# Kernel optimization log

Hardware: AMD Instinct MI355X
Metric: run time of the kernel (lower is better)

Reference implementation:

```python
import jax, jax.numpy as jnp
import numpy as np

NBINS = 256
EARLY_STOP = 0.1  # fraction of nbins with no improvement before early break


def setup_inputs() -> dict:
    key = jax.random.key(0)
    x = jax.random.uniform(key, (8, 3, 1024, 1024), dtype=jnp.float32)
    return {"x": x}


def _otsu_forward(x):
    orig_shape = x.shape
    b, c, h, w = x.shape
    rows = b * c
    xf = x.reshape(rows, h * w)                      # (R, N) one image per row
    N = xf.shape[1]

    # Per-row shift so each row starts at 0 (mirrors `x = (x.T - min_value).T`).
    min_val = xf.min(axis=1, keepdims=True)          # (R, 1)
    xs = xf - min_val
    gmax = xs.max()                                  # global min of xs is 0, global max here
    edges = jnp.linspace(jnp.zeros((), xs.dtype), gmax, NBINS + 1)
    width = gmax / NBINS

    # Per-row histogram with torch.histc semantics over global [0, gmax].
    bin_idx = jnp.clip(jnp.floor(xs / width).astype(jnp.int32), 0, NBINS - 1)
    flat_idx = (jnp.arange(rows, dtype=jnp.int32)[:, None] * NBINS + bin_idx).reshape(-1)
    hist = jnp.bincount(flat_idx, length=rows * NBINS).reshape(rows, NBINS).astype(xs.dtype)
    cum_count = jnp.cumsum(hist, axis=1)             # px_bellow after each bin
    w0 = cum_count / N
    w1 = 1.0 - w0

    # Sorted prefix moments -> subset variances for every threshold in one pass.
    xsort = jnp.sort(xs, axis=1)
    row_mean = xs.mean(axis=1, keepdims=True)
    cvals = xsort - row_mean                         # variance is shift-invariant; centering for stability
    s1 = jnp.cumsum(cvals, axis=1)
    s2 = jnp.cumsum(cvals * cvals, axis=1)
    tot1 = s1[:, -1:]
    tot2 = s2[:, -1:]

    thresh = edges[1:]                               # bin_edges[bin+1], shape (NBINS,)
    # n0[r, bin] = #{xs[r] <= thresh[bin]}  (condition `x <= thresh` in the loop)
    n0 = jax.vmap(lambda row: jnp.searchsorted(row, thresh, side="right"))(xsort)  # (R, NBINS)

    def subset_var(S1, S2, n):
        # unbiased variance (torch.var default); nan for n <= 1 like torch
        nf = n.astype(xs.dtype)
        var = (S2 - S1 * S1 / jnp.maximum(nf, 1.0)) / jnp.maximum(nf - 1.0, 1.0)
        return jnp.where(n > 1, var, jnp.nan)

    idx0 = jnp.maximum(n0 - 1, 0)
    S1_0 = jnp.where(n0 > 0, jnp.take_along_axis(s1, idx0, axis=1), 0.0)
    S2_0 = jnp.where(n0 > 0, jnp.take_along_axis(s2, idx0, axis=1), 0.0)
    mu0 = subset_var(S1_0, S2_0, n0)                 # var of pixels <= thresh
    n1 = N - n0
    mu1 = subset_var(tot1 - S1_0, tot2 - S2_0, n1)   # var of pixels > thresh
    icv = w0 * w1 * (mu0 - mu1) ** 2                 # (R, NBINS)

    # Sequential argmax with the original's global early-stop counter.
    max_try = int(NBINS * EARLY_STOP)

    def step(carry, inputs):
        max_icv, best, no_upd, stopped = carry
        icv_b, t_b = inputs                          # (R,), scalar
        upd = (icv_b > max_icv) & jnp.logical_not(stopped)   # nan > x is False, as in torch
        max_icv = jnp.where(upd, icv_b, max_icv)
        best = jnp.where(upd, t_b, best)
        no_upd = jnp.where(jnp.any(upd), 0, no_upd + 1)
        stopped = stopped | (no_upd >= max_try)
        return (max_icv, best, no_upd, stopped), None

    init = (
        jnp.zeros(rows, xs.dtype),
        jnp.zeros(rows, xs.dtype),
        jnp.zeros((), jnp.int32),
        jnp.zeros((), jnp.bool_),
    )
    (_, best_thresh, _, _), _ = jax.lax.scan(step, init, (icv.T, thresh))

    final_thresh = best_thresh[:, None] + min_val    # back to original scale
    out = jnp.where(xf < final_thresh, jnp.zeros((), xs.dtype), xf)
    return out.reshape(orig_shape)


def reference(x):
    return _otsu_forward(x)
```

## Files before the change

### kernel.cpp

```cpp
#include <hip/hip_runtime.h>
#include <stdint.h>


#define ROWS 24
#define NPIX (1 << 20)
#define NBINS 256
#define BPR 64
#define CHUNK (NPIX / BPR)
#define MAX_TRY 25

typedef float f32x4 __attribute__((ext_vector_type(4)));

static constexpr double kMagic = 6755399441055744.0;
static constexpr double kD1Scale = 17592186044416.0;
static constexpr double kD1Inv = 1.0 / 17592186044416.0;
static constexpr double kD2Scale = 4503599627370496.0;
static constexpr double kD2Inv = 1.0 / 4503599627370496.0;
static constexpr double Nd = 1048576.0;
static constexpr double kEps = 1e-9;

#define OFF_PART  0
#define OFF_FINAL 12288
#define OFF_T32   12544
#define OFF_CNT   16384
#define OFF_COR   40960
#define OFF_D1    65536
#define OFF_D2    114688
#define WS_END    163840

__device__ __forceinline__ void reduce_minmax(const uint2* __restrict__ part,
                                              unsigned* lmn, unsigned* lmx,
                                              int nthreads) {
  int t = threadIdx.x;
  if (t < ROWS) { lmn[t] = 0xFFFFFFFFu; lmx[t] = 0u; }
  __syncthreads();
  for (int p = t; p < ROWS * BPR; p += nthreads) {
    uint2 v = part[p];
    atomicMin(&lmn[p >> 6], v.x);
    atomicMax(&lmx[p >> 6], v.y);
  }
  __syncthreads();
}

__device__ __forceinline__ double compute_w(const unsigned* lmn,
                                            const unsigned* lmx, int t) {
  double d = 0.0;
  if (t < ROWS)
    d = (double)__uint_as_float(lmx[t]) - (double)__uint_as_float(lmn[t]);
  for (int o = 16; o; o >>= 1) d = fmax(d, __shfl_down(d, o));
  return d / 256.0;
}

__global__ __launch_bounds__(256) void k_minmax(const float* __restrict__ x,
                                                uint2* __restrict__ part,
                                                uint4* __restrict__ zero_base) {
  int blk = blockIdx.x;
  if (blk < 36) {
    uint4 z; z.x = 0u; z.y = 0u; z.z = 0u; z.w = 0u;
    zero_base[blk * 256 + threadIdx.x] = z;
  }
  int row = blk / BPR, sub = blk % BPR;
  const float4* p = (const float4*)(x + (size_t)row * NPIX + (size_t)sub * CHUNK);
  float mn = 3.4e38f, mx = 0.0f;
  for (int i = threadIdx.x; i < CHUNK / 4; i += 256) {
    float4 v = p[i];
    mn = fminf(mn, fminf(fminf(v.x, v.y), fminf(v.z, v.w)));
    mx = fmaxf(mx, fmaxf(fmaxf(v.x, v.y), fmaxf(v.z, v.w)));
  }
  __shared__ float smn[4], smx[4];
  for (int o = 32; o; o >>= 1) {
    mn = fminf(mn, __shfl_down(mn, o));
    mx = fmaxf(mx, __shfl_down(mx, o));
  }
  int wave = threadIdx.x >> 6;
  if ((threadIdx.x & 63) == 0) { smn[wave] = mn; smx[wave] = mx; }
  __syncthreads();
  if (threadIdx.x == 0) {
    for (int w = 1; w < 4; ++w) { mn = fminf(mn, smn[w]); mx = fmaxf(mx, smx[w]); }
    uint2 r; r.x = __float_as_uint(mn); r.y = __float_as_uint(mx);
    part[blk] = r;
  }
}

__global__ __launch_bounds__(256) void k_hist(const float* __restrict__ x,
    const uint2* __restrict__ part,
    unsigned* __restrict__ gcnt, int* __restrict__ gcor,
    unsigned long long* __restrict__ gD1, unsigned long long* __restrict__ gD2) {
  __shared__ unsigned lmn[ROWS], lmx[ROWS];
  __shared__ unsigned long long hA[NBINS], hB[NBINS];
  __shared__ int hcor[NBINS];
  __shared__ double s_w, s_rmin;
  int t = threadIdx.x;
  int row = blockIdx.x / BPR, sub = blockIdx.x % BPR;
  hA[t] = 0ull; hB[t] = 0ull; hcor[t] = 0;
  reduce_minmax(part, lmn, lmx, 256);
  if (t < 32) {
    double wv = compute_w(lmn, lmx, t);
    if (t == 0) { s_w = wv; s_rmin = (double)__uint_as_float(lmn[row]); }
  }
  __syncthreads();
  double w = s_w, rmin = s_rmin, rw = 1.0 / w;
  const float4* p = (const float4*)(x + (size_t)row * NPIX + (size_t)sub * CHUNK);
  for (int i = t; i < CHUNK / 4; i += 256) {
    float4 v = p[i];
    float vv[4] = {v.x, v.y, v.z, v.w};
#pragma unroll
    for (int c = 0; c < 4; ++c) {
      double xs = (double)vv[c] - rmin;
      double q1 = xs * rw;
      int b = (int)q1;
      double fr = q1 - (double)b;
      int j; double off;
      if (__builtin_expect(fr >= kEps && fr <= 1.0 - kEps && b <= 255, 1)) {
        j = b; off = (double)b * w;
      } else {
        double q = xs / w;
        b = (int)q; if (b > 255) b = 255;
        double elo = (double)b * w, ehi = (double)(b + 1) * w;
        j = b; off = elo;
        if (xs > ehi) { if (b < 255) { j = b + 1; off = ehi; } }
        else if (b > 0 && xs <= elo) { j = b - 1; off = (double)j * w; }
        if (j != b) { atomicAdd(&hcor[b], 1); atomicAdd(&hcor[j], -1); }
      }
      double delta = xs - off;
      double t1 = fma(delta, kD1Scale, kMagic);
      double dd = delta * delta;
      double t2 = fma(dd, kD2Scale, kMagic);
      unsigned long long d1 = (unsigned long long)__double_as_longlong(t1)
                              & 0x0007FFFFFFFFFFFFull;
      unsigned long long d2 = (unsigned long long)__double_as_longlong(t2)
                              & 0x0007FFFFFFFFFFFFull;
      atomicAdd(&hA[j], d1 | (1ull << 44));
      atomicAdd(&hB[j], d2);
    }
  }
  __syncthreads();
  unsigned long long a = hA[t];
  unsigned c = (unsigned)(a >> 44);
  int base = row * NBINS + t;
  if (c) {
    atomicAdd(&gcnt[base], c);
    atomicAdd(&gD1[base], a & ((1ull << 44) - 1ull));
  }
  if (hB[t]) atomicAdd(&gD2[base], hB[t]);
  if (hcor[t]) atomicAdd(&gcor[base], hcor[t]);
}

__global__ __launch_bounds__(1024) void k_icv_scan(
    const unsigned* __restrict__ gcnt, const int* __restrict__ gcor,
    const unsigned long long* __restrict__ gD1,
    const unsigned long long* __restrict__ gD2,
    const uint2* __restrict__ part,
    double* __restrict__ finalt, float* __restrict__ t32g) {
  __shared__ unsigned lmn[ROWS], lmx[ROWS];
  __shared__ unsigned long long umask[ROWS][4];
  __shared__ unsigned long long ganyw[4];
  __shared__ double s_w;
  __shared__ int s_tstop;
  int t = threadIdx.x;
  if (t < 4) ganyw[t] = 0ull;
  if (t < ROWS * 4) ((unsigned long long*)umask)[t] = 0ull;
  reduce_minmax(part, lmn, lmx, 1024);
  if (t < 32) {
    double wv = compute_w(lmn, lmx, t);
    if (t == 0) s_w = wv;
  }
  __syncthreads();
  double w = s_w;
  int wave = t >> 6, lane = t & 63;
  const double dNAN = __builtin_nan("");

  for (int pass = 0; pass < 2; ++pass) {
    if (pass == 1 && wave >= 8) break;
    int r = pass ? 16 + wave : wave;
    double e1[4], e2[4];
    unsigned long long pc0[4];
#pragma unroll
    for (int k = 0; k < 4; ++k) {
      int bin = k * 64 + lane;
      int idx = r * NBINS + bin;
      unsigned n = gcnt[idx];
      int cor = gcor[idx];
      double d1 = (double)gD1[idx] * kD1Inv;
      double d2v = (double)gD2[idx] * kD2Inv;
      double elo = (double)bin * w;
      e1[k] = (double)n * elo + d1;
      e2[k] = (double)n * (elo * elo) + 2.0 * elo * d1 + d2v;
      pc0[k] = (unsigned long long)n |
               ((unsigned long long)(unsigned)(n + (unsigned)cor) << 32);
    }
    double c1 = 0.0, c2 = 0.0;
    unsigned long long cc = 0ull;
    double E1[4], E2[4];
    unsigned long long CC[4];
#pragma unroll
    for (int k = 0; k < 4; ++k) {
      double p1 = e1[k], p2 = e2[k];
      unsigned long long pc = pc0[k];
      for (int o = 1; o < 64; o <<= 1) {
        double u1 = __shfl_up(p1, o), u2 = __shfl_up(p2, o);
        unsigned long long uc = __shfl_up(pc, o);
        if (lane >= o) { p1 += u1; p2 += u2; pc += uc; }
      }
      E1[k] = p1 + c1; E2[k] = p2 + c2; CC[k] = pc + cc;
      c1 += __shfl(p1, 63); c2 += __shfl(p2, 63); cc += __shfl(pc, 63);
    }
    double total1 = c1, total2 = c2;
    double mean = total1 / Nd;
    double tot1 = total1 - Nd * mean;
    double tot2 = total2 - Nd * mean * mean;
    double icv4[4];
#pragma unroll
    for (int k = 0; k < 4; ++k) {
      unsigned n0i = (unsigned)(CC[k] & 0xffffffffull);
      double n0 = (double)n0i;
      double n1 = Nd - n0;
      double s1raw = E1[k], s2raw = E2[k];
      double S1 = s1raw - n0 * mean;
      double S2 = s2raw - 2.0 * mean * s1raw + n0 * mean * mean;
      double mu0 = (n0i > 1u) ? (S2 - S1 * S1 / n0) / (n0 - 1.0) : dNAN;
      double S1b = tot1 - S1, S2b = tot2 - S2;
      double mu1 = (n1 > 1.0) ? (S2b - S1b * S1b / n1) / (n1 - 1.0) : dNAN;
      double w0 = (double)(unsigned)(CC[k] >> 32) / Nd, w1v = 1.0 - w0;
      double ddv = mu0 - mu1;
      icv4[k] = w0 * w1v * ddv * ddv;
    }
    double m = 0.0;
    unsigned long long myMask[4];
#pragma unroll
    for (int k = 0; k < 4; ++k) {
      double v = icv4[k];
      double pm = v;
      for (int o = 1; o < 64; o <<= 1) {
        double u = __shfl_up(pm, o);
        if (lane >= o) pm = fmax(pm, u);
      }
      double excl = __shfl_up(pm, 1);
      double Mprev = (lane == 0) ? m : fmax(m, excl);
      bool upd = v > Mprev;
      myMask[k] = __ballot(upd);
      m = fmax(m, __shfl(pm, 63));
    }
    if (lane == 0) {
#pragma unroll
      for (int k = 0; k < 4; ++k) {
        umask[r][k] = myMask[k];
        atomicOr(&ganyw[k], myMask[k]);
      }
    }
  }
  __syncthreads();
  if (t == 0) {
    int no_upd = 0, tstop = 255;
    for (int b = 0; b < 256; ++b) {
      bool any = (ganyw[b >> 6] >> (b & 63)) & 1ull;
      if (any) no_upd = 0; else ++no_upd;
      if (no_upd >= MAX_TRY) { tstop = b; break; }
    }
    s_tstop = tstop;
  }
  __syncthreads();
  if (t < ROWS) {
    int tstop = s_tstop;
    int tbest = -1;
    for (int k = 3; k >= 0; --k) {
      unsigned long long msk = umask[t][k];
      int hi = k * 64 + 63;
      if (hi > tstop) {
        int shift = tstop - k * 64;
        if (shift < 0) msk = 0ull;
        else msk &= (shift >= 63) ? ~0ull : ((2ull << shift) - 1ull);
      }
      if (msk) { tbest = k * 64 + 63 - __clzll(msk); break; }
    }
    double rmin = (double)__uint_as_float(lmn[t]);
    double ft = (tbest >= 0) ? (double)(tbest + 1) * w + rmin : rmin;
    finalt[t] = ft;
    float f = (float)ft;
    if ((double)f < ft) f = __uint_as_float(__float_as_uint(f) + 1u);
    t32g[t] = f;
  }
}

__global__ __launch_bounds__(256) void k_out(const float* __restrict__ x,
                                             const float* __restrict__ t32g,
                                             float* __restrict__ out) {
  size_t i = (size_t)blockIdx.x * blockDim.x + threadIdx.x;
  size_t stride = (size_t)gridDim.x * blockDim.x;
  const f32x4* xin = (const f32x4*)x;
  f32x4* o = (f32x4*)out;
  size_t n4 = (size_t)ROWS * NPIX / 4;
  for (; i < n4; i += stride) {
    float ft = t32g[i >> 18];
    f32x4 v = xin[i];
    f32x4 rr;
    rr.x = (v.x < ft) ? 0.0f : v.x;
    rr.y = (v.y < ft) ? 0.0f : v.y;
    rr.z = (v.z < ft) ? 0.0f : v.z;
    rr.w = (v.w < ft) ? 0.0f : v.w;
    __builtin_nontemporal_store(rr, &o[i]);
  }
}

extern "C" void kernel_launch(void* const* d_in, const int* in_sizes, int n_in,
                              void* d_out, int out_size, void* d_ws, size_t ws_size,
                              hipStream_t stream) {
  const float* x = (const float*)d_in[0];
  float* out = (float*)d_out;
  char* ws = (char*)d_ws;
  uint2* part = (uint2*)(ws + OFF_PART);
  double* finalt = (double*)(ws + OFF_FINAL);
  float* t32g = (float*)(ws + OFF_T32);
  unsigned* gcnt = (unsigned*)(ws + OFF_CNT);
  int* gcor = (int*)(ws + OFF_COR);
  unsigned long long* gD1 = (unsigned long long*)(ws + OFF_D1);
  unsigned long long* gD2 = (unsigned long long*)(ws + OFF_D2);

  k_minmax<<<ROWS * BPR, 256, 0, stream>>>(x, part, (uint4*)(ws + OFF_CNT));
  k_hist<<<ROWS * BPR, 256, 0, stream>>>(x, part, gcnt, gcor, gD1, gD2);
  k_icv_scan<<<1, 1024, 0, stream>>>(gcnt, gcor, gD1, gD2, part, finalt, t32g);
  k_out<<<3072, 256, 0, stream>>>(x, t32g, out);
}
```

Baseline: 118.1 us.

## Fuse ICV scan into histogram kernel via last-block ticket, privatize LDS histograms

Removes the separate single-block k_icv_scan launch: the last histogram block (detected through a global atomic done-counter) runs the threshold scan with 256 threads over six row passes. The LDS histograms are replicated per wave to cut atomic contention, the fast-path bin test computes delta directly with an fma, and the output kernel grid shrinks to 2048 blocks. The tail now runs on fewer threads inside a kernel with its own occupancy limits, and correctness depends on the extra zeroed counter and on the fences being ordered correctly.

```diff
diff --git a/kernel.cpp b/kernel.cpp
--- a/kernel.cpp
+++ b/kernel.cpp
@@ -7,6 +7,7 @@
 #define NBINS 256
 #define BPR 64
 #define CHUNK (NPIX / BPR)
+#define NBLK (ROWS * BPR)
 #define MAX_TRY 25
 
 typedef float f32x4 __attribute__((ext_vector_type(4)));
@@ -17,16 +18,22 @@
 static constexpr double kD2Scale = 4503599627370496.0;
 static constexpr double kD2Inv = 1.0 / 4503599627370496.0;
 static constexpr double Nd = 1048576.0;
-static constexpr double kEps = 1e-9;
 
 #define OFF_PART  0
-#define OFF_FINAL 12288
-#define OFF_T32   12544
+#define OFF_T32   12288
 #define OFF_CNT   16384
 #define OFF_COR   40960
 #define OFF_D1    65536
 #define OFF_D2    114688
-#define WS_END    163840
+#define OFF_DONE  163840
+#define ZERO_END  167936
+
+__device__ __forceinline__ unsigned ldg_u32(const unsigned* p) {
+  return __hip_atomic_load(p, __ATOMIC_RELAXED, __HIP_MEMORY_SCOPE_AGENT);
+}
+__device__ __forceinline__ unsigned long long ldg_u64(const unsigned long long* p) {
+  return __hip_atomic_load(p, __ATOMIC_RELAXED, __HIP_MEMORY_SCOPE_AGENT);
+}
 
 __device__ __forceinline__ void reduce_minmax(const uint2* __restrict__ part,
                                               unsigned* lmn, unsigned* lmx,
@@ -34,7 +41,7 @@
   int t = threadIdx.x;
   if (t < ROWS) { lmn[t] = 0xFFFFFFFFu; lmx[t] = 0u; }
   __syncthreads();
-  for (int p = t; p < ROWS * BPR; p += nthreads) {
+  for (int p = t; p < NBLK; p += nthreads) {
     uint2 v = part[p];
     atomicMin(&lmn[p >> 6], v.x);
     atomicMax(&lmx[p >> 6], v.y);
@@ -55,7 +62,7 @@
                                                 uint2* __restrict__ part,
                                                 uint4* __restrict__ zero_base) {
   int blk = blockIdx.x;
-  if (blk < 36) {
+  if (blk < 37) {
     uint4 z; z.x = 0u; z.y = 0u; z.z = 0u; z.w = 0u;
     zero_base[blk * 256 + threadIdx.x] = z;
   }
@@ -82,25 +89,31 @@
   }
 }
 
-__global__ __launch_bounds__(256) void k_hist(const float* __restrict__ x,
+__global__ __launch_bounds__(256, 4) void k_hist(const float* __restrict__ x,
     const uint2* __restrict__ part,
     unsigned* __restrict__ gcnt, int* __restrict__ gcor,
-    unsigned long long* __restrict__ gD1, unsigned long long* __restrict__ gD2) {
+    unsigned long long* __restrict__ gD1, unsigned long long* __restrict__ gD2,
+    unsigned* __restrict__ gdone, float* __restrict__ t32g) {
   __shared__ unsigned lmn[ROWS], lmx[ROWS];
-  __shared__ unsigned long long hA[NBINS], hB[NBINS];
+  __shared__ unsigned long long hA[4][NBINS], hB[4][NBINS];
   __shared__ int hcor[NBINS];
   __shared__ double s_w, s_rmin;
   int t = threadIdx.x;
   int row = blockIdx.x / BPR, sub = blockIdx.x % BPR;
-  hA[t] = 0ull; hB[t] = 0ull; hcor[t] = 0;
+  int wavei = t >> 6, lane = t & 63;
+#pragma unroll
+  for (int wv = 0; wv < 4; ++wv) { hA[wv][t] = 0ull; hB[wv][t] = 0ull; }
+  hcor[t] = 0;
   reduce_minmax(part, lmn, lmx, 256);
-  if (t < 32) {
+  if (t < 64) {
     double wv = compute_w(lmn, lmx, t);
     if (t == 0) { s_w = wv; s_rmin = (double)__uint_as_float(lmn[row]); }
   }
   __syncthreads();
   double w = s_w, rmin = s_rmin, rw = 1.0 / w;
+  double lo_eps = w * 1e-9, hi_eps = w * (1.0 - 1e-9);
   const float4* p = (const float4*)(x + (size_t)row * NPIX + (size_t)sub * CHUNK);
+#pragma unroll 2
   for (int i = t; i < CHUNK / 4; i += 256) {
     float4 v = p[i];
     float vv[4] = {v.x, v.y, v.z, v.w};
@@ -109,81 +122,68 @@
       double xs = (double)vv[c] - rmin;
       double q1 = xs * rw;
       int b = (int)q1;
-      double fr = q1 - (double)b;
-      int j; double off;
-      if (__builtin_expect(fr >= kEps && fr <= 1.0 - kEps && b <= 255, 1)) {
-        j = b; off = (double)b * w;
-      } else {
+      double delta = fma(-(double)b, w, xs);
+      int j = b;
+      if (__builtin_expect(!(delta >= lo_eps) | !(delta <= hi_eps) | (b > 255), 0)) {
         double q = xs / w;
         b = (int)q; if (b > 255) b = 255;
         double elo = (double)b * w, ehi = (double)(b + 1) * w;
-        j = b; off = elo;
+        j = b; double off = elo;
         if (xs > ehi) { if (b < 255) { j = b + 1; off = ehi; } }
         else if (b > 0 && xs <= elo) { j = b - 1; off = (double)j * w; }
         if (j != b) { atomicAdd(&hcor[b], 1); atomicAdd(&hcor[j], -1); }
-      }
-      double delta = xs - off;
+        delta = xs - off;
+      }
       double t1 = fma(delta, kD1Scale, kMagic);
-      double dd = delta * delta;
-      double t2 = fma(dd, kD2Scale, kMagic);
+      double t2 = fma(delta * delta, kD2Scale, kMagic);
       unsigned long long d1 = (unsigned long long)__double_as_longlong(t1)
                               & 0x0007FFFFFFFFFFFFull;
       unsigned long long d2 = (unsigned long long)__double_as_longlong(t2)
                               & 0x0007FFFFFFFFFFFFull;
-      atomicAdd(&hA[j], d1 | (1ull << 44));
-      atomicAdd(&hB[j], d2);
-    }
-  }
-  __syncthreads();
-  unsigned long long a = hA[t];
+      atomicAdd(&hA[wavei][j], d1 | (1ull << 44));
+      atomicAdd(&hB[wavei][j], d2);
+    }
+  }
+  __syncthreads();
+  unsigned long long a = hA[0][t] + hA[1][t] + hA[2][t] + hA[3][t];
+  unsigned long long b2 = hB[0][t] + hB[1][t] + hB[2][t] + hB[3][t];
   unsigned c = (unsigned)(a >> 44);
   int base = row * NBINS + t;
   if (c) {
     atomicAdd(&gcnt[base], c);
     atomicAdd(&gD1[base], a & ((1ull << 44) - 1ull));
   }
-  if (hB[t]) atomicAdd(&gD2[base], hB[t]);
+  if (b2) atomicAdd(&gD2[base], b2);
   if (hcor[t]) atomicAdd(&gcor[base], hcor[t]);
-}
-
-__global__ __launch_bounds__(1024) void k_icv_scan(
-    const unsigned* __restrict__ gcnt, const int* __restrict__ gcor,
-    const unsigned long long* __restrict__ gD1,
-    const unsigned long long* __restrict__ gD2,
-    const uint2* __restrict__ part,
-    double* __restrict__ finalt, float* __restrict__ t32g) {
-  __shared__ unsigned lmn[ROWS], lmx[ROWS];
+
+  __threadfence();
+  __syncthreads();
+  __shared__ unsigned s_last;
+  if (t == 0) s_last = (atomicAdd(gdone, 1u) == NBLK - 1) ? 1u : 0u;
+  __syncthreads();
+  if (!s_last) return;
+  __threadfence();
+
   __shared__ unsigned long long umask[ROWS][4];
   __shared__ unsigned long long ganyw[4];
-  __shared__ double s_w;
   __shared__ int s_tstop;
-  int t = threadIdx.x;
   if (t < 4) ganyw[t] = 0ull;
-  if (t < ROWS * 4) ((unsigned long long*)umask)[t] = 0ull;
-  reduce_minmax(part, lmn, lmx, 1024);
-  if (t < 32) {
-    double wv = compute_w(lmn, lmx, t);
-    if (t == 0) s_w = wv;
-  }
-  __syncthreads();
-  double w = s_w;
-  int wave = t >> 6, lane = t & 63;
+  __syncthreads();
   const double dNAN = __builtin_nan("");
-
-  for (int pass = 0; pass < 2; ++pass) {
-    if (pass == 1 && wave >= 8) break;
-    int r = pass ? 16 + wave : wave;
+  double wv2 = s_w;
+  for (int pass = 0; pass < 6; ++pass) {
+    int r = pass * 4 + wavei;
     double e1[4], e2[4];
     unsigned long long pc0[4];
 #pragma unroll
     for (int k = 0; k < 4; ++k) {
       int bin = k * 64 + lane;
       int idx = r * NBINS + bin;
-      unsigned n = gcnt[idx];
-      int cor = gcor[idx];
-      double d1 = (double)gD1[idx] * kD1Inv;
-      double d2v = (double)gD2[idx] * kD2Inv;
-      double elo = (double)bin * w;
+      unsigned n = ldg_u32(&gcnt[idx]);
+      int cor = (int)ldg_u32((const unsigned*)&gcor[idx]);
+      double d1 = (double)ldg_u64(&gD1[idx]) * kD1Inv;
+      double d2v = (double)ldg_u64(&gD2[idx]) * kD2Inv;
+      double elo = (double)bin * wv2;
       e1[k] = (double)n * elo + d1;
       e2[k] = (double)n * (elo * elo) + 2.0 * elo * d1 + d2v;
       pc0[k] = (unsigned long long)n |
@@ -274,8 +274,7 @@
       if (msk) { tbest = k * 64 + 63 - __clzll(msk); break; }
     }
     double rmin = (double)__uint_as_float(lmn[t]);
-    double ft = (tbest >= 0) ? (double)(tbest + 1) * w + rmin : rmin;
-    finalt[t] = ft;
+    double ft = (tbest >= 0) ? (double)(tbest + 1) * wv2 + rmin : rmin;
     float f = (float)ft;
     if ((double)f < ft) f = __uint_as_float(__float_as_uint(f) + 1u);
     t32g[t] = f;
@@ -309,15 +308,14 @@
   float* out = (float*)d_out;
   char* ws = (char*)d_ws;
   uint2* part = (uint2*)(ws + OFF_PART);
-  double* finalt = (double*)(ws + OFF_FINAL);
   float* t32g = (float*)(ws + OFF_T32);
   unsigned* gcnt = (unsigned*)(ws + OFF_CNT);
   int* gcor = (int*)(ws + OFF_COR);
   unsigned long long* gD1 = (unsigned long long*)(ws + OFF_D1);
   unsigned long long* gD2 = (unsigned long long*)(ws + OFF_D2);
-
-  k_minmax<<<ROWS * BPR, 256, 0, stream>>>(x, part, (uint4*)(ws + OFF_CNT));
-  k_hist<<<ROWS * BPR, 256, 0, stream>>>(x, part, gcnt, gcor, gD1, gD2);
-  k_icv_scan<<<1, 1024, 0, stream>>>(gcnt, gcor, gD1, gD2, part, finalt, t32g);
-  k_out<<<3072, 256, 0, stream>>>(x, t32g, out);
-}
+  unsigned* gdone = (unsigned*)(ws + OFF_DONE);
+
+  k_minmax<<<NBLK, 256, 0, stream>>>(x, part, (uint4*)(ws + OFF_CNT));
+  k_hist<<<NBLK, 256, 0, stream>>>(x, part, gcnt, gcor, gD1, gD2, gdone, t32g);
+  k_out<<<2048, 256, 0, stream>>>(x, t32g, out);
+}
```

Measured after the change: 246.8 us. +109.0%, slower.
